# Performance work log

Measured on AMD Instinct MI355X. Metric: run time of the kernel, lower is better.

The kernel has to match this reference:

```python
import jax, jax.numpy as jnp
import numpy as np

B, S, D = 2, 2048, 2048
H, KVH, HD = 16, 4, 128
M = 2  # modalities
THETA = 10000.0
REP = H // KVH


def make_freq_cis(seq_len, head_dim, theta):
    # (S, head_dim//2, 2, 2) rotation matrices [[cos,-sin],[sin,cos]]
    inv = theta ** (-jnp.arange(0, head_dim, 2, dtype=jnp.float32) / head_dim)
    ang = jnp.arange(seq_len, dtype=jnp.float32)[:, None] * inv[None, :]  # (S, hd/2)
    c, s = jnp.cos(ang), jnp.sin(ang)
    row0 = jnp.stack([c, -s], axis=-1)
    row1 = jnp.stack([s, c], axis=-1)
    return jnp.stack([row0, row1], axis=-2)  # (S, hd/2, 2, 2)


def setup_inputs() -> dict:
    key = jax.random.key(0)
    ks = jax.random.split(key, 7)
    std = D ** -0.5
    x = jax.random.normal(ks[0], (B, S, D), dtype=jnp.float32)
    freq_cis = make_freq_cis(S, HD, THETA)
    modality_ids = jax.random.randint(ks[1], (B, S), 0, M, dtype=jnp.int32)
    wq = jax.random.normal(ks[2], (M, D, H * HD), dtype=jnp.float32) * std
    wk = jax.random.normal(ks[3], (M, D, KVH * HD), dtype=jnp.float32) * std
    wv = jax.random.normal(ks[4], (M, D, KVH * HD), dtype=jnp.float32) * std
    wo = jax.random.normal(ks[5], (M, H * HD, D), dtype=jnp.float32) * std
    return {"x": x, "freq_cis": freq_cis, "modality_ids": modality_ids,
            "wq": wq, "wk": wk, "wv": wv, "wo": wo}


def apply_rope(t, freq_cis):
    # t: (B, S, h, HD); freq_cis: (S, HD//2, 2, 2)
    b, s, h, hd = t.shape
    t2 = t.reshape(b, s, h, hd // 2, 2)
    out = jnp.einsum('bshdk,sdjk->bshdj', t2, freq_cis)
    return out.reshape(b, s, h, hd)


def reference(x, freq_cis, modality_ids, wq, wk, wv, wo):
    bsz, seq, dim = x.shape
    onehot = jax.nn.one_hot(modality_ids, M, dtype=x.dtype)  # (B,S,M)
    # per-modality QKV projection, then combine (masks partition tokens)
    q = jnp.einsum('bsm,bsd,mdo->bso', onehot, x, wq).reshape(bsz, seq, H, HD)
    k = jnp.einsum('bsm,bsd,mdo->bso', onehot, x, wk).reshape(bsz, seq, KVH, HD)
    v = jnp.einsum('bsm,bsd,mdo->bso', onehot, x, wv).reshape(bsz, seq, KVH, HD)
    q = apply_rope(q, freq_cis)
    k = apply_rope(k, freq_cis)
    # GQA: repeat_interleave kv heads along head dim
    k = jnp.repeat(k, REP, axis=2)
    v = jnp.repeat(v, REP, axis=2)
    scale = 1.0 / jnp.sqrt(jnp.asarray(HD, dtype=x.dtype))
    scores = jnp.einsum('bqhd,bkhd->bhqk', q, k) * scale
    causal = jnp.tril(jnp.ones((seq, seq), dtype=bool))
    scores = jnp.where(causal[None, None], scores, jnp.finfo(x.dtype).min)
    probs = jax.nn.softmax(scores, axis=-1)
    attn = jnp.einsum('bhqk,bkhd->bqhd', probs, v).reshape(bsz, seq, H * HD)
    # per-modality output projection
    out = jnp.einsum('bsm,bso,moe->bse', onehot, attn, wo)
    return out
```

## Files before the change

kernel.cpp:

```cpp
#include <hip/hip_runtime.h>
#include <stdint.h>

typedef unsigned short u16;
typedef __bf16  bf16x8 __attribute__((ext_vector_type(8), may_alias));
typedef u16     u16x8  __attribute__((ext_vector_type(8), may_alias));
typedef float   f32x4  __attribute__((ext_vector_type(4)));
typedef float   f32x4u __attribute__((ext_vector_type(4), may_alias));

#define Bv   2
#define Sv   2048
#define Dv   2048
#define Hv   16
#define KVHv 4
#define HDv  128
#define Tv   (Bv*Sv)
#define QKVN 3072
#define MAXROWS 4352

__device__ __forceinline__ float b2f(u16 u) {
    union { float f; uint32_t i; } x; x.i = ((uint32_t)u) << 16; return x.f;
}
__device__ __forceinline__ u16 f2b(float f) {
    union { float f; uint32_t u; } x; x.f = f;
    uint32_t r = x.u + 0x7fff + ((x.u >> 16) & 1);
    return (u16)(r >> 16);
}
__device__ __forceinline__ void gload_lds16(const void* g, void* l) {
    __builtin_amdgcn_global_load_lds((__attribute__((address_space(1))) void*)(uintptr_t)g,
                                     (__attribute__((address_space(3))) void*)(uintptr_t)l,
                                     16, 0, 0);
}

__global__ __launch_bounds__(1024) void scan_mod(const int* __restrict__ mod, int* __restrict__ fwd,
                                                 int* __restrict__ inv, int* __restrict__ hdr) {
    __shared__ int cnt[1024];
    const int tid = threadIdx.x;
    int m[4]; int c = 0;
#pragma unroll
    for (int e = 0; e < 4; ++e) { m[e] = mod[tid * 4 + e]; c += (m[e] == 0); }
    cnt[tid] = c;
    __syncthreads();
    for (int off = 1; off < 1024; off <<= 1) {
        int v = (tid >= off) ? cnt[tid - off] : 0;
        __syncthreads();
        cnt[tid] += v;
        __syncthreads();
    }
    const int c0 = cnt[1023];
    const int c0pad = (c0 + 255) & ~255;
    const int c1 = Tv - c0;
    const int total = c0pad + ((c1 + 255) & ~255);
    for (int p = tid; p < MAXROWS; p += 1024) inv[p] = -1;
    __syncthreads();
    const int ex0 = cnt[tid] - c;
    int z = 0;
#pragma unroll
    for (int e = 0; e < 4; ++e) {
        int t = tid * 4 + e;
        int pos;
        if (m[e] == 0) { pos = ex0 + z; ++z; }
        else           { pos = c0pad + (t - (ex0 + z)); }
        fwd[t] = pos;
        inv[pos] = t;
    }
    if (tid == 0) { hdr[0] = total >> 8; hdr[1] = c0pad; hdr[2] = total; }
}

__global__ void gather_cast(const float* __restrict__ x, const int* __restrict__ inv,
                            u16* __restrict__ Xg) {
    int v = blockIdx.x * 256 + threadIdx.x;
    int pos = v >> 8, c8 = (v & 255) * 8;
    int t = inv[pos];
    u16x8 val = {0, 0, 0, 0, 0, 0, 0, 0};
    if (t >= 0) {
        f32x4u a = *(const f32x4u*)&x[(size_t)t * Dv + c8];
        f32x4u b = *(const f32x4u*)&x[(size_t)t * Dv + c8 + 4];
#pragma unroll
        for (int j = 0; j < 4; ++j) { val[j] = f2b(a[j]); val[4 + j] = f2b(b[j]); }
    }
    *(u16x8*)&Xg[(size_t)pos * Dv + c8] = val;
}

__global__ void gather_rows(const u16* __restrict__ O, const int* __restrict__ inv,
                            u16* __restrict__ Ag) {
    int pos = blockIdx.x;
    int c8 = threadIdx.x * 8;
    int t = inv[pos];
    u16x8 val = {0, 0, 0, 0, 0, 0, 0, 0};
    if (t >= 0) val = *(const u16x8*)&O[(size_t)t * 2048 + c8];
    *(u16x8*)&Ag[(size_t)pos * 2048 + c8] = val;
}

__global__ void transpose_cast(const float* __restrict__ in, u16* __restrict__ out, int C,
                               size_t inZ, size_t outZ) {
    in  += (size_t)blockIdx.z * inZ;
    out += (size_t)blockIdx.z * outZ;
    __shared__ u16 tile[64][72];
    const int tr = blockIdx.y * 64, tc = blockIdx.x * 64;
    const int tid = threadIdx.x;
#pragma unroll
    for (int i = 0; i < 4; ++i) {
        int s = tid + 256 * i;
        int r = s >> 4, c4 = (s & 15) * 4;
        f32x4u v = *(const f32x4u*)&in[(size_t)(tr + r) * C + tc + c4];
#pragma unroll
        for (int j = 0; j < 4; ++j) tile[r][c4 + j] = f2b(v[j]);
    }
    __syncthreads();
#pragma unroll
    for (int i = 0; i < 2; ++i) {
        int s = tid + 256 * i;
        int r = s >> 3, c8 = (s & 7) * 8;
        u16x8 v;
#pragma unroll
        for (int j = 0; j < 8; ++j) v[j] = tile[c8 + j][r];
        *(u16x8*)&out[(size_t)(tc + r) * 2048 + tr + c8] = v;
    }
}

__device__ __forceinline__ void store_c(u16* C, size_t idx, float v) { C[idx] = f2b(v); }
__device__ __forceinline__ void store_c(float* C, size_t idx, float v) { C[idx] = v; }

template <typename OutT>
__global__ __launch_bounds__(512, 2) void gemm256(const u16* __restrict__ A,
                                                  const u16* __restrict__ Bt,
                                                  OutT* __restrict__ C,
                                                  const int* __restrict__ inv,
                                                  const int* __restrict__ hdr,
                                                  int Nfull, int ldC) {
    const int total = hdr[2], c0pad = hdr[1];
    const int bm = blockIdx.y * 256;
    if (bm >= total) return;
    const u16* B = Bt + (size_t)((bm >= c0pad) ? 1 : 0) * Nfull * 2048;
    const int bn = blockIdx.x * 256;
    const int tid = threadIdx.x;
    const int wave = tid >> 6, lane = tid & 63;
    const int l15 = lane & 15, l4 = lane >> 4;
    const int wm = wave >> 2;
    const int wn = wave & 3;
    const int bhh = wn >> 1, brr = (wn & 1) * 64;
    const int rsw = l15 & 7;
    __shared__ u16 ldsA[2][2][128 * 64];
    __shared__ u16 ldsB[2][2][128 * 64];
    const int srow = tid >> 3;
    const int ssw  = (tid & 7) ^ (srow & 7);
    const int wofs = wave * 8 * 64;

    f32x4 acc[8][4] = {};

    auto stA = [&](int sl, int h, int jrb, int kt) {
        gload_lds16(A + (size_t)(bm + h * 128 + jrb * 64 + srow) * 2048 + kt * 64 + ssw * 8,
                    &ldsA[sl][h][jrb * 64 * 64 + wofs]);
    };
    auto stB = [&](int sl, int h, int jrb, int kt) {
        gload_lds16(B + (size_t)(bn + h * 128 + jrb * 64 + srow) * 2048 + kt * 64 + ssw * 8,
                    &ldsB[sl][h][jrb * 64 * 64 + wofs]);
    };

    stB(0, 0, 0, 0); stB(0, 0, 1, 0); stB(0, 1, 0, 0); stB(0, 1, 1, 0);
    stA(0, 0, 0, 0); stA(0, 1, 0, 0); stA(0, 0, 1, 0); stA(0, 1, 1, 0);
    asm volatile("s_waitcnt vmcnt(2)" ::: "memory");
    __builtin_amdgcn_s_barrier();
    __builtin_amdgcn_sched_barrier(0);

    for (int kt = 0; kt < 32; ++kt) {
        const int s = kt & 1;
        const bool st = (kt < 31);
        bf16x8 bfr[4][2];
#pragma unroll
        for (int fj = 0; fj < 4; ++fj)
#pragma unroll
            for (int kc = 0; kc < 2; ++kc)
                bfr[fj][kc] = *(const bf16x8*)&ldsB[s][bhh][(brr + fj * 16 + l15) * 64 + ((kc * 4 + l4) ^ rsw) * 8];
#pragma unroll
        for (int q = 0; q < 4; ++q) {
            bf16x8 af[2][2];
#pragma unroll
            for (int fi = 0; fi < 2; ++fi)
#pragma unroll
                for (int kc = 0; kc < 2; ++kc)
                    af[fi][kc] = *(const bf16x8*)&ldsA[s][wm][(q * 32 + fi * 16 + l15) * 64 + ((kc * 4 + l4) ^ rsw) * 8];
            if (st) {
                if      (q == 0) { stB(s ^ 1, 0, 0, kt + 1); stB(s ^ 1, 0, 1, kt + 1); }
                else if (q == 1) { stB(s ^ 1, 1, 0, kt + 1); stB(s ^ 1, 1, 1, kt + 1); }
                else if (q == 2) { stA(s ^ 1, 0, 0, kt + 1); stA(s ^ 1, 1, 0, kt + 1); }
                else             { stA(s ^ 1, 0, 1, kt + 1); stA(s ^ 1, 1, 1, kt + 1); }
            }
            __builtin_amdgcn_s_setprio(1);
#pragma unroll
            for (int kc = 0; kc < 2; ++kc)
#pragma unroll
                for (int fi = 0; fi < 2; ++fi)
#pragma unroll
                    for (int fj = 0; fj < 4; ++fj)
                        acc[q * 2 + fi][fj] = __builtin_amdgcn_mfma_f32_16x16x32_bf16(
                            af[fi][kc], bfr[fj][kc], acc[q * 2 + fi][fj], 0, 0, 0);
            __builtin_amdgcn_s_setprio(0);
            if (q == 1) {
                if (st) asm volatile("s_waitcnt vmcnt(4)" ::: "memory");
                else    asm volatile("s_waitcnt vmcnt(0)" ::: "memory");
                __builtin_amdgcn_sched_barrier(0);
            }
            if (q == 3 && st) {
                asm volatile("s_waitcnt vmcnt(2)" ::: "memory");
                __builtin_amdgcn_sched_barrier(0);
            }
            __builtin_amdgcn_s_barrier();
            __builtin_amdgcn_sched_barrier(0);
        }
    }
#pragma unroll
    for (int fi = 0; fi < 8; ++fi)
#pragma unroll
        for (int r = 0; r < 4; ++r) {
            int row = bm + wm * 128 + fi * 16 + l4 * 4 + r;
            int t = inv[row];
            if (t >= 0) {
#pragma unroll
                for (int fj = 0; fj < 4; ++fj) {
                    int col = bn + wn * 64 + fj * 16 + l15;
                    store_c(C, (size_t)t * ldC + col, acc[fi][fj][r]);
                }
            }
        }
}

__global__ void rope_kernel(u16* __restrict__ QKV, const float* __restrict__ fc) {
    int p = blockIdx.x * 256 + threadIdx.x;
    const int t = p / 1280;
    const int r = p - t * 1280;
    const int s = t & (Sv - 1);
    int col, d2; float scale;
    if (r < 1024) { col = 2 * r;                d2 = r & 63;  scale = 0.08838834764831845f; }
    else          { int rr = r - 1024; col = 2048 + 2 * rr; d2 = rr & 63; scale = 1.0f; }
    u16* ptr = QKV + (size_t)t * QKVN + col;
    float t0 = b2f(ptr[0]), t1 = b2f(ptr[1]);
    f32x4u f = *(const f32x4u*)&fc[((size_t)s * 64 + d2) * 4];
    ptr[0] = f2b((t0 * f[0] + t1 * f[1]) * scale);
    ptr[1] = f2b((t0 * f[2] + t1 * f[3]) * scale);
}

__global__ __launch_bounds__(512) void attn_fwd(const u16* __restrict__ QKV, u16* __restrict__ O) {
    const int p = blockIdx.x;
    const int h = blockIdx.y, b = blockIdx.z;
    const int kvh = h >> 2;
    const int tid = threadIdx.x, wave = tid >> 6, lane = tid & 63;
    const int wgrp = wave >> 2, wl = wave & 3;
    const int l15 = lane & 15, l4 = lane >> 4;
    const int myqb = wgrp ? (31 - p) : p;
    __shared__ u16 Kb[2][64 * 128];
    __shared__ u16 Vb[2][128 * 64];
    __shared__ u16 Pl[8][16 * 64];

    bf16x8 qf[4];
    {
        const size_t qrow = (size_t)(b * Sv + myqb * 64 + wl * 16 + l15);
#pragma unroll
        for (int kc = 0; kc < 4; ++kc)
            qf[kc] = *(const bf16x8*)&QKV[qrow * QKVN + h * 128 + kc * 32 + l4 * 8];
    }
    f32x4 oacc[8] = {};
    float mrow = -1e30f;
    float lrow = 0.f;

    const size_t kvbase = (size_t)b * Sv * QKVN + 2048 + kvh * 128;

    {
#pragma unroll
        for (int i = 0; i < 2; ++i) {
            int s_u = wave * 64 + 512 * i;
            int s = s_u + lane;
            int r = s >> 4;
            int cs = (s & 15) ^ (r & 7);
            gload_lds16(QKV + kvbase + (size_t)r * QKVN + cs * 8, &Kb[0][(size_t)s_u * 8]);
        }
        u16x8 vr0 = *(const u16x8*)&QKV[kvbase + 512 + (size_t)lane * QKVN + (0 * 8 + wave) * 8];
        u16x8 vr1 = *(const u16x8*)&QKV[kvbase + 512 + (size_t)lane * QKVN + (1 * 8 + wave) * 8];
#pragma unroll
        for (int jj = 0; jj < 8; ++jj) {
            int d0 = wave * 8 + jj, d1 = (8 + wave) * 8 + jj;
            Vb[0][d0 * 64 + ((((lane >> 3) ^ jj) << 3) | (lane & 7))] = vr0[jj];
            Vb[0][d1 * 64 + ((((lane >> 3) ^ jj) << 3) | (lane & 7))] = vr1[jj];
        }
    }
    __syncthreads();

    for (int j = 0; j < 32; ++j) {
        const int cur = j & 1;
        const bool stage_next = (j < 31);
        u16x8 vn0, vn1;
        if (stage_next) {
            const size_t nb = kvbase + (size_t)(j + 1) * 64 * QKVN;
#pragma unroll
            for (int i = 0; i < 2; ++i) {
                int s_u = wave * 64 + 512 * i;
                int s = s_u + lane;
                int r = s >> 4;
                int cs = (s & 15) ^ (r & 7);
                gload_lds16(QKV + nb + (size_t)r * QKVN + cs * 8, &Kb[cur ^ 1][(size_t)s_u * 8]);
            }
            vn0 = *(const u16x8*)&QKV[nb + 512 + (size_t)lane * QKVN + (0 * 8 + wave) * 8];
            vn1 = *(const u16x8*)&QKV[nb + 512 + (size_t)lane * QKVN + (1 * 8 + wave) * 8];
        }
        if (j <= myqb) {
            f32x4 sacc[4] = {};
#pragma unroll
            for (int kc = 0; kc < 4; ++kc)
#pragma unroll
                for (int nt = 0; nt < 4; ++nt) {
                    int cs = ((kc * 4 + l4) ^ (l15 & 7));
                    bf16x8 kf = *(const bf16x8*)&Kb[cur][(nt * 16 + l15) * 128 + cs * 8];
                    sacc[nt] = __builtin_amdgcn_mfma_f32_16x16x32_bf16(kf, qf[kc], sacc[nt], 0, 0, 0);
                }
            if (j == myqb) {
#pragma unroll
                for (int nt = 0; nt < 4; ++nt)
#pragma unroll
                    for (int r = 0; r < 4; ++r)
                        if (nt * 16 + l4 * 4 + r > wl * 16 + l15)
                            sacc[nt][r] = -1e30f;
            }
            f32x4 mv = sacc[0];
#pragma unroll
            for (int nt = 1; nt < 4; ++nt)
#pragma unroll
                for (int r = 0; r < 4; ++r) mv[r] = fmaxf(mv[r], sacc[nt][r]);
            float mx = fmaxf(fmaxf(mv[0], mv[1]), fmaxf(mv[2], mv[3]));
            mx = fmaxf(mx, __shfl_xor(mx, 16, 64));
            mx = fmaxf(mx, __shfl_xor(mx, 32, 64));
            float mnew = fmaxf(mrow, mx);
            float fs = __expf(mrow - mnew);
            mrow = mnew;
            f32x4 pv = {0.f, 0.f, 0.f, 0.f};
#pragma unroll
            for (int nt = 0; nt < 4; ++nt)
#pragma unroll
                for (int r = 0; r < 4; ++r) {
                    float pe = __expf(sacc[nt][r] - mnew);
                    sacc[nt][r] = pe;
                    pv[r] += pe;
                }
            float ps = (pv[0] + pv[1]) + (pv[2] + pv[3]);
            ps += __shfl_xor(ps, 16, 64);
            ps += __shfl_xor(ps, 32, 64);
            lrow = lrow * fs + ps;
            float fsq[4];
#pragma unroll
            for (int r = 0; r < 4; ++r) fsq[r] = __shfl(fs, l4 * 4 + r, 64);
#pragma unroll
            for (int nt = 0; nt < 8; ++nt)
#pragma unroll
                for (int r = 0; r < 4; ++r) oacc[nt][r] *= fsq[r];
#pragma unroll
            for (int nt = 0; nt < 4; ++nt)
#pragma unroll
                for (int r = 0; r < 4; ++r) {
                    int kv = nt * 16 + l4 * 4 + r;
                    Pl[wave][l15 * 64 + ((((kv >> 3) ^ (l15 & 7)) << 3) | (kv & 7))] = f2b(sacc[nt][r]);
                }
            bf16x8 pf0 = *(const bf16x8*)&Pl[wave][l15 * 64 + ((l4 ^ (l15 & 7)) << 3)];
            bf16x8 pf1 = *(const bf16x8*)&Pl[wave][l15 * 64 + (((4 + l4) ^ (l15 & 7)) << 3)];
#pragma unroll
            for (int nt = 0; nt < 8; ++nt) {
                int d = nt * 16 + l15;
                bf16x8 v0 = *(const bf16x8*)&Vb[cur][d * 64 + ((l4 ^ (l15 & 7)) << 3)];
                bf16x8 v1 = *(const bf16x8*)&Vb[cur][d * 64 + (((4 + l4) ^ (l15 & 7)) << 3)];
                oacc[nt] = __builtin_amdgcn_mfma_f32_16x16x32_bf16(pf0, v0, oacc[nt], 0, 0, 0);
                oacc[nt] = __builtin_amdgcn_mfma_f32_16x16x32_bf16(pf1, v1, oacc[nt], 0, 0, 0);
            }
        }
        if (stage_next) {
#pragma unroll
            for (int jj = 0; jj < 8; ++jj) {
                int d0 = wave * 8 + jj, d1 = (8 + wave) * 8 + jj;
                Vb[cur ^ 1][d0 * 64 + ((((lane >> 3) ^ jj) << 3) | (lane & 7))] = vn0[jj];
                Vb[cur ^ 1][d1 * 64 + ((((lane >> 3) ^ jj) << 3) | (lane & 7))] = vn1[jj];
            }
        }
        __syncthreads();
    }
    float lrq[4];
#pragma unroll
    for (int r = 0; r < 4; ++r) lrq[r] = __shfl(lrow, l4 * 4 + r, 64);
#pragma unroll
    for (int nt = 0; nt < 8; ++nt)
#pragma unroll
        for (int r = 0; r < 4; ++r) {
            int qg = myqb * 64 + wl * 16 + l4 * 4 + r;
            O[(size_t)(b * Sv + qg) * 2048 + h * 128 + nt * 16 + l15] = f2b(oacc[nt][r] / lrq[r]);
        }
}

extern "C" void kernel_launch(void* const* d_in, const int* in_sizes, int n_in,
                              void* d_out, int out_size, void* d_ws, size_t ws_size,
                              hipStream_t stream) {
    const float* x   = (const float*)d_in[0];
    const float* fc  = (const float*)d_in[1];
    const int*   mod = (const int*)d_in[2];
    const float* wq  = (const float*)d_in[3];
    const float* wk  = (const float*)d_in[4];
    const float* wv  = (const float*)d_in[5];
    const float* wo  = (const float*)d_in[6];
    float* out = (float*)d_out;
    char* ws = (char*)d_ws;
    u16* Wqkv_t = (u16*)(ws);
    u16* Wo_t   = (u16*)(ws + 25165824);
    u16* Xg     = (u16*)(ws + 41943040);
    u16* QKV    = (u16*)(ws + 59768832);
    int* fwd    = (int*)(ws + 84934656);
    int* inv    = (int*)(ws + 84951040);
    int* hdr    = (int*)(ws + 84968448);
    u16* Ag     = Xg;
    u16* O      = (u16*)(ws);

    transpose_cast<<<dim3(32, 32, 2), 256, 0, stream>>>(wq, Wqkv_t, 2048,
        (size_t)2048 * 2048, (size_t)3072 * 2048);
    transpose_cast<<<dim3(8, 32, 2),  256, 0, stream>>>(wk, Wqkv_t + (size_t)2048 * 2048, 512,
        (size_t)2048 * 512,  (size_t)3072 * 2048);
    transpose_cast<<<dim3(8, 32, 2),  256, 0, stream>>>(wv, Wqkv_t + (size_t)2560 * 2048, 512,
        (size_t)2048 * 512,  (size_t)3072 * 2048);
    transpose_cast<<<dim3(32, 32, 2), 256, 0, stream>>>(wo, Wo_t, 2048,
        (size_t)2048 * 2048, (size_t)2048 * 2048);
    scan_mod<<<1, 1024, 0, stream>>>(mod, fwd, inv, hdr);
    gather_cast<<<MAXROWS, 256, 0, stream>>>(x, inv, Xg);
    gemm256<u16><<<dim3(12, 17), 512, 0, stream>>>(Xg, Wqkv_t, QKV, inv, hdr, 3072, 3072);
    rope_kernel<<<20480, 256, 0, stream>>>(QKV, fc);
    attn_fwd<<<dim3(16, 16, 2), 512, 0, stream>>>(QKV, O);
    gather_rows<<<MAXROWS, 256, 0, stream>>>(O, inv, Ag);
    gemm256<float><<<dim3(8, 17), 512, 0, stream>>>(Ag, Wo_t, out, inv, hdr, 2048, 2048);
}
```

Measured before the change: 243.3 us.

## Fuse attention output scatter into attn epilogue and keep P in registers

Removes the gather_rows kernel: the attention epilogue writes normalized output rows straight into the modality-sorted Ag buffer through the fwd map, staged via shared memory for coalesced 16-byte stores. K rows are loaded in a permuted order so the transposed MFMA (V as A operand, P as B) lets the exp'd scores be packed to bf16 in registers with v_cvt_pk_bf16_f32, dropping the per-wave LDS round trip for P and the per-row shuffles for the rescale factor. The softmax switches to exp2f, with log2(e) folded into the Q scale applied in rope. It relies on fwd mapping every token to its padded row, and the register and shared-memory layout changes carry correctness risk.

```diff
diff --git a/kernel.cpp b/kernel.cpp
--- a/kernel.cpp
+++ b/kernel.cpp
@@ -79,16 +79,6 @@
         for (int j = 0; j < 4; ++j) { val[j] = f2b(a[j]); val[4 + j] = f2b(b[j]); }
     }
     *(u16x8*)&Xg[(size_t)pos * Dv + c8] = val;
-}
-
-__global__ void gather_rows(const u16* __restrict__ O, const int* __restrict__ inv,
-                            u16* __restrict__ Ag) {
-    int pos = blockIdx.x;
-    int c8 = threadIdx.x * 8;
-    int t = inv[pos];
-    u16x8 val = {0, 0, 0, 0, 0, 0, 0, 0};
-    if (t >= 0) val = *(const u16x8*)&O[(size_t)t * 2048 + c8];
-    *(u16x8*)&Ag[(size_t)pos * 2048 + c8] = val;
 }
 
 __global__ void transpose_cast(const float* __restrict__ in, u16* __restrict__ out, int C,
@@ -231,7 +221,7 @@
     const int r = p - t * 1280;
     const int s = t & (Sv - 1);
     int col, d2; float scale;
-    if (r < 1024) { col = 2 * r;                d2 = r & 63;  scale = 0.08838834764831845f; }
+    if (r < 1024) { col = 2 * r;                d2 = r & 63;  scale = 0.12751742f; }
     else          { int rr = r - 1024; col = 2048 + 2 * rr; d2 = rr & 63; scale = 1.0f; }
     u16* ptr = QKV + (size_t)t * QKVN + col;
     float t0 = b2f(ptr[0]), t1 = b2f(ptr[1]);
@@ -240,7 +230,8 @@
     ptr[1] = f2b((t0 * f[2] + t1 * f[3]) * scale);
 }
 
-__global__ __launch_bounds__(512) void attn_fwd(const u16* __restrict__ QKV, u16* __restrict__ O) {
+__global__ __launch_bounds__(512) void attn_fwd(const u16* __restrict__ QKV, u16* __restrict__ Ag,
+                                                const int* __restrict__ fwd) {
     const int p = blockIdx.x;
     const int h = blockIdx.y, b = blockIdx.z;
     const int kvh = h >> 2;
@@ -248,9 +239,7 @@
     const int wgrp = wave >> 2, wl = wave & 3;
     const int l15 = lane & 15, l4 = lane >> 4;
     const int myqb = wgrp ? (31 - p) : p;
-    __shared__ u16 Kb[2][64 * 128];
-    __shared__ u16 Vb[2][128 * 64];
-    __shared__ u16 Pl[8][16 * 64];
+    __shared__ u16 smem[32768];
 
     bf16x8 qf[4];
     {
@@ -271,16 +260,17 @@
             int s_u = wave * 64 + 512 * i;
             int s = s_u + lane;
             int r = s >> 4;
+            int kvsrc = (r & 32) | ((r & 12) << 1) | ((r & 16) >> 2) | (r & 3);
             int cs = (s & 15) ^ (r & 7);
-            gload_lds16(QKV + kvbase + (size_t)r * QKVN + cs * 8, &Kb[0][(size_t)s_u * 8]);
+            gload_lds16(QKV + kvbase + (size_t)kvsrc * QKVN + cs * 8, &smem[(size_t)s_u * 8]);
         }
         u16x8 vr0 = *(const u16x8*)&QKV[kvbase + 512 + (size_t)lane * QKVN + (0 * 8 + wave) * 8];
         u16x8 vr1 = *(const u16x8*)&QKV[kvbase + 512 + (size_t)lane * QKVN + (1 * 8 + wave) * 8];
 #pragma unroll
         for (int jj = 0; jj < 8; ++jj) {
             int d0 = wave * 8 + jj, d1 = (8 + wave) * 8 + jj;
-            Vb[0][d0 * 64 + ((((lane >> 3) ^ jj) << 3) | (lane & 7))] = vr0[jj];
-            Vb[0][d1 * 64 + ((((lane >> 3) ^ jj) << 3) | (lane & 7))] = vr1[jj];
+            smem[16384 + d0 * 64 + ((((lane >> 3) ^ jj) << 3) | (lane & 7))] = vr0[jj];
+            smem[16384 + d1 * 64 + ((((lane >> 3) ^ jj) << 3) | (lane & 7))] = vr1[jj];
         }
     }
     __syncthreads();
@@ -288,6 +278,10 @@
     for (int j = 0; j < 32; ++j) {
         const int cur = j & 1;
         const bool stage_next = (j < 31);
+        u16* Kcur = smem + cur * 8192;
+        u16* Knxt = smem + (cur ^ 1) * 8192;
+        u16* Vcur = smem + 16384 + cur * 8192;
+        u16* Vnxt = smem + 16384 + (cur ^ 1) * 8192;
         u16x8 vn0, vn1;
         if (stage_next) {
             const size_t nb = kvbase + (size_t)(j + 1) * 64 * QKVN;
@@ -296,8 +290,9 @@
                 int s_u = wave * 64 + 512 * i;
                 int s = s_u + lane;
                 int r = s >> 4;
+                int kvsrc = (r & 32) | ((r & 12) << 1) | ((r & 16) >> 2) | (r & 3);
                 int cs = (s & 15) ^ (r & 7);
-                gload_lds16(QKV + nb + (size_t)r * QKVN + cs * 8, &Kb[cur ^ 1][(size_t)s_u * 8]);
+                gload_lds16(QKV + nb + (size_t)kvsrc * QKVN + cs * 8, &Knxt[(size_t)s_u * 8]);
             }
             vn0 = *(const u16x8*)&QKV[nb + 512 + (size_t)lane * QKVN + (0 * 8 + wave) * 8];
             vn1 = *(const u16x8*)&QKV[nb + 512 + (size_t)lane * QKVN + (1 * 8 + wave) * 8];
@@ -309,7 +304,7 @@
 #pragma unroll
                 for (int nt = 0; nt < 4; ++nt) {
                     int cs = ((kc * 4 + l4) ^ (l15 & 7));
-                    bf16x8 kf = *(const bf16x8*)&Kb[cur][(nt * 16 + l15) * 128 + cs * 8];
+                    bf16x8 kf = *(const bf16x8*)&Kcur[(nt * 16 + l15) * 128 + cs * 8];
                     sacc[nt] = __builtin_amdgcn_mfma_f32_16x16x32_bf16(kf, qf[kc], sacc[nt], 0, 0, 0);
                 }
             if (j == myqb) {
@@ -317,7 +312,7 @@
                 for (int nt = 0; nt < 4; ++nt)
 #pragma unroll
                     for (int r = 0; r < 4; ++r)
-                        if (nt * 16 + l4 * 4 + r > wl * 16 + l15)
+                        if ((nt >> 1) * 32 + l4 * 8 + (nt & 1) * 4 + r > wl * 16 + l15)
                             sacc[nt][r] = -1e30f;
             }
             f32x4 mv = sacc[0];
@@ -329,14 +324,14 @@
             mx = fmaxf(mx, __shfl_xor(mx, 16, 64));
             mx = fmaxf(mx, __shfl_xor(mx, 32, 64));
             float mnew = fmaxf(mrow, mx);
-            float fs = __expf(mrow - mnew);
+            float fs = exp2f(mrow - mnew);
             mrow = mnew;
             f32x4 pv = {0.f, 0.f, 0.f, 0.f};
 #pragma unroll
             for (int nt = 0; nt < 4; ++nt)
 #pragma unroll
                 for (int r = 0; r < 4; ++r) {
-                    float pe = __expf(sacc[nt][r] - mnew);
+                    float pe = exp2f(sacc[nt][r] - mnew);
                     sacc[nt][r] = pe;
                     pv[r] += pe;
                 }
@@ -344,51 +339,55 @@
             ps += __shfl_xor(ps, 16, 64);
             ps += __shfl_xor(ps, 32, 64);
             lrow = lrow * fs + ps;
-            float fsq[4];
-#pragma unroll
-            for (int r = 0; r < 4; ++r) fsq[r] = __shfl(fs, l4 * 4 + r, 64);
 #pragma unroll
             for (int nt = 0; nt < 8; ++nt)
 #pragma unroll
-                for (int r = 0; r < 4; ++r) oacc[nt][r] *= fsq[r];
-#pragma unroll
-            for (int nt = 0; nt < 4; ++nt)
-#pragma unroll
-                for (int r = 0; r < 4; ++r) {
-                    int kv = nt * 16 + l4 * 4 + r;
-                    Pl[wave][l15 * 64 + ((((kv >> 3) ^ (l15 & 7)) << 3) | (kv & 7))] = f2b(sacc[nt][r]);
-                }
-            bf16x8 pf0 = *(const bf16x8*)&Pl[wave][l15 * 64 + ((l4 ^ (l15 & 7)) << 3)];
-            bf16x8 pf1 = *(const bf16x8*)&Pl[wave][l15 * 64 + (((4 + l4) ^ (l15 & 7)) << 3)];
+                for (int r = 0; r < 4; ++r) oacc[nt][r] *= fs;
+            union { uint32_t w[4]; bf16x8 v; } pb0u, pb1u;
+#pragma unroll
+            for (int nt = 0; nt < 2; ++nt) {
+                asm("v_cvt_pk_bf16_f32 %0, %1, %2" : "=v"(pb0u.w[nt * 2])     : "v"(sacc[nt][0]), "v"(sacc[nt][1]));
+                asm("v_cvt_pk_bf16_f32 %0, %1, %2" : "=v"(pb0u.w[nt * 2 + 1]) : "v"(sacc[nt][2]), "v"(sacc[nt][3]));
+                asm("v_cvt_pk_bf16_f32 %0, %1, %2" : "=v"(pb1u.w[nt * 2])     : "v"(sacc[nt + 2][0]), "v"(sacc[nt + 2][1]));
+                asm("v_cvt_pk_bf16_f32 %0, %1, %2" : "=v"(pb1u.w[nt * 2 + 1]) : "v"(sacc[nt + 2][2]), "v"(sacc[nt + 2][3]));
+            }
+            bf16x8 pb0 = pb0u.v, pb1 = pb1u.v;
 #pragma unroll
             for (int nt = 0; nt < 8; ++nt) {
                 int d = nt * 16 + l15;
-                bf16x8 v0 = *(const bf16x8*)&Vb[cur][d * 64 + ((l4 ^ (l15 & 7)) << 3)];
-                bf16x8 v1 = *(const bf16x8*)&Vb[cur][d * 64 + (((4 + l4) ^ (l15 & 7)) << 3)];
-                oacc[nt] = __builtin_amdgcn_mfma_f32_16x16x32_bf16(pf0, v0, oacc[nt], 0, 0, 0);
-                oacc[nt] = __builtin_amdgcn_mfma_f32_16x16x32_bf16(pf1, v1, oacc[nt], 0, 0, 0);
+                bf16x8 v0 = *(const bf16x8*)&Vcur[d * 64 + ((l4 ^ (l15 & 7)) << 3)];
+                bf16x8 v1 = *(const bf16x8*)&Vcur[d * 64 + (((4 + l4) ^ (l15 & 7)) << 3)];
+                oacc[nt] = __builtin_amdgcn_mfma_f32_16x16x32_bf16(v0, pb0, oacc[nt], 0, 0, 0);
+                oacc[nt] = __builtin_amdgcn_mfma_f32_16x16x32_bf16(v1, pb1, oacc[nt], 0, 0, 0);
             }
         }
         if (stage_next) {
 #pragma unroll
             for (int jj = 0; jj < 8; ++jj) {
                 int d0 = wave * 8 + jj, d1 = (8 + wave) * 8 + jj;
-                Vb[cur ^ 1][d0 * 64 + ((((lane >> 3) ^ jj) << 3) | (lane & 7))] = vn0[jj];
-                Vb[cur ^ 1][d1 * 64 + ((((lane >> 3) ^ jj) << 3) | (lane & 7))] = vn1[jj];
+                Vnxt[d0 * 64 + ((((lane >> 3) ^ jj) << 3) | (lane & 7))] = vn0[jj];
+                Vnxt[d1 * 64 + ((((lane >> 3) ^ jj) << 3) | (lane & 7))] = vn1[jj];
             }
         }
         __syncthreads();
     }
-    float lrq[4];
-#pragma unroll
-    for (int r = 0; r < 4; ++r) lrq[r] = __shfl(lrow, l4 * 4 + r, 64);
-#pragma unroll
-    for (int nt = 0; nt < 8; ++nt)
-#pragma unroll
-        for (int r = 0; r < 4; ++r) {
-            int qg = myqb * 64 + wl * 16 + l4 * 4 + r;
-            O[(size_t)(b * Sv + qg) * 2048 + h * 128 + nt * 16 + l15] = f2b(oacc[nt][r] / lrq[r]);
-        }
+    {
+        u16* epi = smem + wave * (16 * 136);
+        float rinv = 1.0f / lrow;
+#pragma unroll
+        for (int nt = 0; nt < 8; ++nt)
+#pragma unroll
+            for (int r = 0; r < 4; ++r)
+                epi[l15 * 136 + nt * 16 + l4 * 4 + r] = f2b(oacc[nt][r] * rinv);
+        const int q = lane >> 2;
+        const int rowmap = fwd[b * Sv + myqb * 64 + wl * 16 + q];
+#pragma unroll
+        for (int it = 0; it < 4; ++it) {
+            int dv = (lane & 3) + it * 4;
+            u16x8 v = *(const u16x8*)&epi[q * 136 + dv * 8];
+            *(u16x8*)&Ag[(size_t)rowmap * 2048 + h * 128 + dv * 8] = v;
+        }
+    }
 }
 
 extern "C" void kernel_launch(void* const* d_in, const int* in_sizes, int n_in,
@@ -411,7 +410,6 @@
     int* inv    = (int*)(ws + 84951040);
     int* hdr    = (int*)(ws + 84968448);
     u16* Ag     = Xg;
-    u16* O      = (u16*)(ws);
 
     transpose_cast<<<dim3(32, 32, 2), 256, 0, stream>>>(wq, Wqkv_t, 2048,
         (size_t)2048 * 2048, (size_t)3072 * 2048);
@@ -425,7 +423,6 @@
     gather_cast<<<MAXROWS, 256, 0, stream>>>(x, inv, Xg);
     gemm256<u16><<<dim3(12, 17), 512, 0, stream>>>(Xg, Wqkv_t, QKV, inv, hdr, 3072, 3072);
     rope_kernel<<<20480, 256, 0, stream>>>(QKV, fc);
-    attn_fwd<<<dim3(16, 16, 2), 512, 0, stream>>>(QKV, O);
-    gather_rows<<<MAXROWS, 256, 0, stream>>>(O, inv, Ag);
+    attn_fwd<<<dim3(16, 16, 2), 512, 0, stream>>>(QKV, Ag, fwd);
     gemm256<float><<<dim3(8, 17), 512, 0, stream>>>(Ag, Wo_t, out, inv, hdr, 2048, 2048);
 }
```

After: 230.9 us. -5.1%, faster.
